# Optimization experiments

Measured on AMD Instinct MI355X. Metric: run time of the kernel, lower is better.

The kernel has to match this reference:

```python
import jax, jax.numpy as jnp
import numpy as np

VERY_NEG = -1e30


def setup_inputs() -> dict:
    key = jax.random.key(0)
    k1, k2, k3, k4, k5 = jax.random.split(key, 5)
    T, J, B, D = 1024, 128, 32, 256
    context = jax.random.normal(k1, (T, B, D), dtype=jnp.float32)
    question = jax.random.normal(k2, (J, B, D), dtype=jnp.float32)
    con_lens = jax.random.randint(k3, (B,), 1, T + 1)
    qu_lens = jax.random.randint(k4, (B,), 1, J + 1)
    # learned trilinear weight (3*D, 1), small init like uniform weight init
    att_w = jax.random.normal(k5, (3 * D, 1), dtype=jnp.float32) * 0.05
    return {"context": context, "question": question, "con_lens": con_lens,
            "qu_lens": qu_lens, "att_w": att_w}


def reference(context, question, con_lens, qu_lens, att_w):
    T, B, D = context.shape
    J = question.shape[0]
    # Decompose trilinear score: [c, q, c*q] @ att_w = c.w_c + q.w_q + (c*q).w_cq
    w_c, w_q, w_cq = att_w[:D, 0], att_w[D:2 * D, 0], att_w[2 * D:, 0]
    c_proj = jnp.einsum('tbd,d->bt', context, w_c)            # (B,T)
    q_proj = jnp.einsum('jbd,d->bj', question, w_q)           # (B,J)
    cross = jnp.einsum('tbd,jbd->btj', context * w_cq, question)  # (B,T,J)
    S = c_proj[:, :, None] + q_proj[:, None, :] + cross       # (B,T,J)
    # exp_mask: valid (t < con_len) & (j < qu_len), invalid += VERY_NEG
    t_valid = jnp.arange(T)[None, :] < con_lens[:, None]      # (B,T)
    j_valid = jnp.arange(J)[None, :] < qu_lens[:, None]       # (B,J)
    valid = t_valid[:, :, None] & j_valid[:, None, :]         # (B,T,J)
    S = S + jnp.where(valid, 0.0, VERY_NEG)
    # context-to-query attention
    c2q_w = jax.nn.softmax(S, axis=-1)                        # (B,T,J)
    question_bt = jnp.transpose(question, (1, 0, 2))          # (B,J,D)
    c2q = jnp.einsum('btj,bjd->btd', c2q_w, question_bt)      # (B,T,D)
    # query-to-context attention: rows of the expanded bmm are identical,
    # so compute the weighted sum once and broadcast (same math as expand+bmm)
    value = jax.nn.softmax(jnp.max(S, axis=2), axis=-1)       # (B,T)
    context_bt = jnp.transpose(context, (1, 0, 2))            # (B,T,D)
    q2c_vec = jnp.einsum('bt,btd->bd', value, context_bt)     # (B,D)
    q2c = jnp.broadcast_to(q2c_vec[:, None, :], (B, T, D))
    G = jnp.concatenate([context_bt, c2q, context_bt * c2q, context_bt * q2c],
                        axis=2)                               # (B,T,4D)
    # zero out padded context positions
    G = G * t_valid[:, :, None].astype(G.dtype)
    return G
```

## Files before the change

### kernel.cpp

```cpp
#include <hip/hip_runtime.h>
#include <hip/hip_bf16.h>

#define T_ 1024
#define J_ 128
#define B_ 32
#define D_ 256
#define VERY_NEG (-1e30f)

using u16 = unsigned short;
typedef __bf16 bf16x8 __attribute__((ext_vector_type(8)));
typedef u16 u16x8 __attribute__((ext_vector_type(8)));
typedef u16 u16x4 __attribute__((ext_vector_type(4)));
typedef float f32x4 __attribute__((ext_vector_type(4)));

__device__ __forceinline__ float bf2f(u16 u) {
  union { unsigned int i; float f; } v; v.i = ((unsigned int)u) << 16; return v.f;
}
__device__ __forceinline__ u16 f2bf(float f) {
  union { float f; unsigned int i; } v; v.f = f;
  unsigned int i = v.i;
  return (u16)((i + 0x7fffu + ((i >> 16) & 1u)) >> 16);
}

__global__ __launch_bounds__(256) void k_prep(const float* __restrict__ qst,
                                              const float* __restrict__ attw,
                                              float* __restrict__ ws_qproj,
                                              u16* __restrict__ ws_qbf) {
  const int wave = threadIdx.x >> 6, lane = threadIdx.x & 63;
  const int gid = blockIdx.x * 4 + wave;
  const int b = gid >> 7, j = gid & 127;
  const size_t off = (size_t)j * (B_ * D_) + b * D_ + lane * 4;
  f32x4 a = *(const f32x4*)(qst + off);
  f32x4 w = *(const f32x4*)(attw + D_ + lane * 4);
  u16x4 qb;
#pragma unroll
  for (int e = 0; e < 4; ++e) qb[e] = f2bf(a[e]);
  *(u16x4*)(ws_qbf + off) = qb;
  float s = a[0] * w[0] + a[1] * w[1] + a[2] * w[2] + a[3] * w[3];
#pragma unroll
  for (int m = 32; m >= 1; m >>= 1) s += __shfl_xor(s, m);
  if (lane == 0) ws_qproj[gid] = s;
}

__global__ __launch_bounds__(256) void k_main(const float* __restrict__ ctx,
                                              const u16* __restrict__ qbf,
                                              const int* __restrict__ con_lens,
                                              const int* __restrict__ qu_lens,
                                              const float* __restrict__ attw,
                                              const float* __restrict__ ws_qproj,
                                              float* __restrict__ ws_mtile,
                                              float* __restrict__ ws_pden,
                                              float* __restrict__ ws_pnum,
                                              float* __restrict__ out) {
  __shared__ __align__(16) u16 smem[24576];
  __shared__ float mrow_l[64];
  __shared__ float msc[1];
  u16* qtl = smem;
  u16* plds = smem + 16384;
  u16* c2q_l = smem;
  float* red4 = (float*)(smem + 16896);

  const int tid = threadIdx.x;
  const int wave = tid >> 6, lane = tid & 63;
  const int lrow = lane & 15, lgrp = lane >> 4;
  const int b = blockIdx.y;
  const int t0 = blockIdx.x * 64;
  const int t0w = t0 + wave * 16;
  const int con = con_lens[b], qu = qu_lens[b];

  f32x4 accS[8];
#pragma unroll
  for (int jb = 0; jb < 8; ++jb) accS[jb] = f32x4{0.f, 0.f, 0.f, 0.f};

  float cpr = 0.f;
  const float* rowAp = ctx + (size_t)(t0w + lrow) * (B_ * D_) + b * D_;
#pragma unroll
  for (int ks = 0; ks < 8; ++ks) {
    const int d0 = ks * 32 + lgrp * 8;
    f32x4 a0 = *(const f32x4*)(rowAp + d0);
    f32x4 a1 = *(const f32x4*)(rowAp + d0 + 4);
    f32x4 wq0 = *(const f32x4*)(attw + 2 * D_ + d0);
    f32x4 wq1 = *(const f32x4*)(attw + 2 * D_ + d0 + 4);
    f32x4 wc0 = *(const f32x4*)(attw + d0);
    f32x4 wc1 = *(const f32x4*)(attw + d0 + 4);
    bf16x8 afrag;
#pragma unroll
    for (int e = 0; e < 4; ++e) {
      afrag[e] = (__bf16)(a0[e] * wq0[e]);
      afrag[4 + e] = (__bf16)(a1[e] * wq1[e]);
      cpr += a0[e] * wc0[e] + a1[e] * wc1[e];
    }
#pragma unroll
    for (int jb = 0; jb < 8; ++jb) {
      const bf16x8 bfrag =
          *(const bf16x8*)(qbf + (size_t)(jb * 16 + lrow) * (B_ * D_) + b * D_ + d0);
      accS[jb] = __builtin_amdgcn_mfma_f32_16x16x32_bf16(afrag, bfrag, accS[jb], 0, 0, 0);
    }
  }
  cpr += __shfl_xor(cpr, 16);
  cpr += __shfl_xor(cpr, 32);

  float cp[4];
#pragma unroll
  for (int r = 0; r < 4; ++r) cp[r] = __shfl(cpr, lgrp * 4 + r);
  float qp[8];
#pragma unroll
  for (int jb = 0; jb < 8; ++jb) qp[jb] = ws_qproj[b * 128 + jb * 16 + lrow];

  float mx[4] = {-3e38f, -3e38f, -3e38f, -3e38f};
#pragma unroll
  for (int jb = 0; jb < 8; ++jb) {
    const int j = jb * 16 + lrow;
#pragma unroll
    for (int r = 0; r < 4; ++r) {
      const int t = t0w + lgrp * 4 + r;
      float s = accS[jb][r] + cp[r] + qp[jb];
      if (t >= con || j >= qu) s += VERY_NEG;
      accS[jb][r] = s;
      mx[r] = fmaxf(mx[r], s);
    }
  }
#pragma unroll
  for (int r = 0; r < 4; ++r) {
    mx[r] = fmaxf(mx[r], __shfl_xor(mx[r], 1));
    mx[r] = fmaxf(mx[r], __shfl_xor(mx[r], 2));
    mx[r] = fmaxf(mx[r], __shfl_xor(mx[r], 4));
    mx[r] = fmaxf(mx[r], __shfl_xor(mx[r], 8));
  }
  if (lrow == 0) {
#pragma unroll
    for (int r = 0; r < 4; ++r) mrow_l[wave * 16 + lgrp * 4 + r] = mx[r];
  }
  float sm[4] = {0.f, 0.f, 0.f, 0.f};
#pragma unroll
  for (int jb = 0; jb < 8; ++jb)
#pragma unroll
    for (int r = 0; r < 4; ++r) {
      float p = __expf(accS[jb][r] - mx[r]);
      accS[jb][r] = p;
      sm[r] += p;
    }
#pragma unroll
  for (int r = 0; r < 4; ++r) {
    sm[r] += __shfl_xor(sm[r], 1);
    sm[r] += __shfl_xor(sm[r], 2);
    sm[r] += __shfl_xor(sm[r], 4);
    sm[r] += __shfl_xor(sm[r], 8);
  }

  {
    u16* pl = plds + wave * 2048;
#pragma unroll
    for (int r = 0; r < 4; ++r) {
      const float inv = 1.0f / sm[r];
      const int m = lgrp * 4 + r;
#pragma unroll
      for (int jb = 0; jb < 8; ++jb) {
        const int n = jb * 16 + lrow;
        pl[m * 128 + (((n >> 3) ^ m) << 3) + (n & 7)] = f2bf(accS[jb][r] * inv);
      }
    }
  }

  f32x4 accO[16];
#pragma unroll
  for (int nb = 0; nb < 16; ++nb) accO[nb] = f32x4{0.f, 0.f, 0.f, 0.f};

#pragma unroll
  for (int h = 0; h < 2; ++h) {
    __syncthreads();
    for (int it = 0; it < 8; ++it) {
      const int task = it * 256 + tid;
      const int j = task & 127, dblk = task >> 7;
      u16x8 q = *(const u16x8*)(qbf + (size_t)j * (B_ * D_) + b * D_ + h * 128 + dblk * 8);
#pragma unroll
      for (int e = 0; e < 8; ++e) {
        const int dl = dblk * 8 + e;
        qtl[dl * 128 + (((j >> 3) ^ (dl & 15)) << 3) + (j & 7)] = q[e];
      }
    }
    __syncthreads();
#pragma unroll
    for (int ks2 = 0; ks2 < 4; ++ks2) {
      const int chunkA = ks2 * 4 + lgrp;
      const bf16x8 ap =
          *(const bf16x8*)(plds + wave * 2048 + lrow * 128 + ((chunkA ^ lrow) << 3));
#pragma unroll
      for (int nbl = 0; nbl < 8; ++nbl) {
        const int dl = nbl * 16 + lrow;
        const bf16x8 bq = *(const bf16x8*)(qtl + dl * 128 + ((chunkA ^ (dl & 15)) << 3));
        accO[h * 8 + nbl] =
            __builtin_amdgcn_mfma_f32_16x16x32_bf16(ap, bq, accO[h * 8 + nbl], 0, 0, 0);
      }
    }
  }
  __syncthreads();

#pragma unroll
  for (int nb = 0; nb < 16; ++nb)
#pragma unroll
    for (int r = 0; r < 4; ++r) {
      const int row = wave * 16 + lgrp * 4 + r;
      const int d = nb * 16 + lrow;
      c2q_l[row * 264 + d] = f2bf(accO[nb][r]);
    }
  __syncthreads();

  if (tid < 64) {
    float v = mrow_l[tid];
#pragma unroll
    for (int m = 32; m >= 1; m >>= 1) v = fmaxf(v, __shfl_xor(v, m));
    if (tid == 0) msc[0] = v;
  }
  __syncthreads();
  const float Mt = msc[0];
  if (tid < 64) {
    const float mr = mrow_l[tid];
    const float e = (mr < -1e29f) ? 0.f : __expf(mr - Mt);
    mrow_l[tid] = e;
    float s2 = e;
#pragma unroll
    for (int m = 32; m >= 1; m >>= 1) s2 += __shfl_xor(s2, m);
    if (tid == 0) {
      ws_mtile[b * 16 + blockIdx.x] = Mt;
      ws_pden[b * 16 + blockIdx.x] = s2;
    }
  }
  __syncthreads();

  f32x4 acc4 = {0.f, 0.f, 0.f, 0.f};
  const int c = tid & 63;
  for (int ii = 0; ii < 16; ++ii) {
    const int row = ii * 4 + wave;
    const int t = t0 + row;
    const bool valid = t < con;
    f32x4 cr = *(const f32x4*)(ctx + (size_t)t * (B_ * D_) + b * D_ + c * 4);
    u16x4 cq = *(const u16x4*)(c2q_l + row * 264 + c * 4);
    const float w = mrow_l[row];
    f32x4 p0, p1, p2;
#pragma unroll
    for (int e = 0; e < 4; ++e) {
      const float cf = valid ? cr[e] : 0.f;
      const float qf = valid ? bf2f(cq[e]) : 0.f;
      p0[e] = cf;
      p1[e] = qf;
      p2[e] = cf * qf;
      acc4[e] += w * cr[e];
    }
    float* g = out + ((size_t)(b * 1024 + t)) * 1024 + c * 4;
    *(f32x4*)(g) = p0;
    *(f32x4*)(g + 256) = p1;
    *(f32x4*)(g + 512) = p2;
  }
  *(f32x4*)(red4 + wave * 256 + c * 4) = acc4;
  __syncthreads();
  {
    const float sum = red4[tid] + red4[256 + tid] + red4[512 + tid] + red4[768 + tid];
    ws_pnum[((size_t)b * 16 + blockIdx.x) * 256 + tid] = sum;
  }
}

__global__ __launch_bounds__(256) void k_combine(const float* __restrict__ ws_mtile,
                                                 const float* __restrict__ ws_pden,
                                                 const float* __restrict__ ws_pnum,
                                                 float* __restrict__ q2c) {
  __shared__ float se[16];
  __shared__ float sden[1];
  const int b = blockIdx.x, tid = threadIdx.x;
  if (tid < 64) {
    const float mt = (tid < 16) ? ws_mtile[b * 16 + tid] : -3e38f;
    float M = mt;
#pragma unroll
    for (int m = 8; m >= 1; m >>= 1) M = fmaxf(M, __shfl_xor(M, m));
    const float pd = (tid < 16) ? ws_pden[b * 16 + tid] : 0.f;
    const float e = (tid < 16 && mt > -1e29f) ? __expf(mt - M) : 0.f;
    if (tid < 16) se[tid] = e;
    float cden = e * pd;
#pragma unroll
    for (int m = 8; m >= 1; m >>= 1) cden += __shfl_xor(cden, m);
    if (tid == 0) sden[0] = cden;
  }
  __syncthreads();
  const float den = sden[0];
  float num = 0.f;
#pragma unroll
  for (int i = 0; i < 16; ++i) num += se[i] * ws_pnum[((size_t)b * 16 + i) * 256 + tid];
  q2c[b * 256 + tid] = num / den;
}

__global__ __launch_bounds__(256) void k_part3(const float* __restrict__ ctx,
                                               const int* __restrict__ con_lens,
                                               const float* __restrict__ q2c,
                                               float* __restrict__ out) {
  const int idx = blockIdx.x * 256 + threadIdx.x;
  const int c = idx & 63, t = (idx >> 6) & 1023, b = idx >> 16;
  const bool valid = t < con_lens[b];
  f32x4 cr = *(const f32x4*)(ctx + (size_t)t * (B_ * D_) + b * D_ + c * 4);
  const f32x4 qv = *(const f32x4*)(q2c + b * D_ + c * 4);
  f32x4 o;
#pragma unroll
  for (int e = 0; e < 4; ++e) o[e] = valid ? cr[e] * qv[e] : 0.f;
  *(f32x4*)(out + ((size_t)(b * 1024 + t)) * 1024 + 768 + c * 4) = o;
}

extern "C" void kernel_launch(void* const* d_in, const int* in_sizes, int n_in,
                              void* d_out, int out_size, void* d_ws, size_t ws_size,
                              hipStream_t stream) {
  const float* ctx = (const float*)d_in[0];
  const float* qst = (const float*)d_in[1];
  const int* con = (const int*)d_in[2];
  const int* qu = (const int*)d_in[3];
  const float* attw = (const float*)d_in[4];
  float* out = (float*)d_out;

  float* ws = (float*)d_ws;
  float* ws_qproj = ws;
  u16* ws_qbf = (u16*)(ws + 4096);
  float* ws_mtile = ws + 528384;
  float* ws_pden = ws + 528896;
  float* ws_pnum = ws + 529408;
  float* ws_q2c = ws + 660480;

  k_prep<<<1024, 256, 0, stream>>>(qst, attw, ws_qproj, ws_qbf);
  k_main<<<dim3(16, 32), 256, 0, stream>>>(ctx, ws_qbf, con, qu, attw, ws_qproj,
                                           ws_mtile, ws_pden, ws_pnum, out);
  k_combine<<<32, 256, 0, stream>>>(ws_mtile, ws_pden, ws_pnum, ws_q2c);
  k_part3<<<8192, 256, 0, stream>>>(ctx, con, ws_q2c, out);
}
```

Measured before the change: 190.7 us.

## Fuse all stages into one kernel with per-batch spin barriers

Merges prep, main, combine and the q2c output pass into a single persistent kernel. Per-batch global atomic counters act as barriers between the 16 blocks of each batch. Context rows stay in registers so the q2c output columns are written without re-reading ctx, and three kernel launches go away. The cost is a memset per call, spin-wait barriers that depend on all 512 blocks being co-resident (launch bounds 256,2), and more register pressure from caching 16 f32x4 values.

```diff
diff --git a/kernel.cpp b/kernel.cpp
--- a/kernel.cpp
+++ b/kernel.cpp
@@ -22,39 +22,32 @@
   return (u16)((i + 0x7fffu + ((i >> 16) & 1u)) >> 16);
 }
 
-__global__ __launch_bounds__(256) void k_prep(const float* __restrict__ qst,
-                                              const float* __restrict__ attw,
-                                              float* __restrict__ ws_qproj,
-                                              u16* __restrict__ ws_qbf) {
-  const int wave = threadIdx.x >> 6, lane = threadIdx.x & 63;
-  const int gid = blockIdx.x * 4 + wave;
-  const int b = gid >> 7, j = gid & 127;
-  const size_t off = (size_t)j * (B_ * D_) + b * D_ + lane * 4;
-  f32x4 a = *(const f32x4*)(qst + off);
-  f32x4 w = *(const f32x4*)(attw + D_ + lane * 4);
-  u16x4 qb;
-#pragma unroll
-  for (int e = 0; e < 4; ++e) qb[e] = f2bf(a[e]);
-  *(u16x4*)(ws_qbf + off) = qb;
-  float s = a[0] * w[0] + a[1] * w[1] + a[2] * w[2] + a[3] * w[3];
-#pragma unroll
-  for (int m = 32; m >= 1; m >>= 1) s += __shfl_xor(s, m);
-  if (lane == 0) ws_qproj[gid] = s;
-}
-
-__global__ __launch_bounds__(256) void k_main(const float* __restrict__ ctx,
-                                              const u16* __restrict__ qbf,
-                                              const int* __restrict__ con_lens,
-                                              const int* __restrict__ qu_lens,
-                                              const float* __restrict__ attw,
-                                              const float* __restrict__ ws_qproj,
-                                              float* __restrict__ ws_mtile,
-                                              float* __restrict__ ws_pden,
-                                              float* __restrict__ ws_pnum,
-                                              float* __restrict__ out) {
+__device__ __forceinline__ void b_barrier(int* cnt, int tid) {
+  __threadfence();
+  __syncthreads();
+  if (tid == 0) {
+    __hip_atomic_fetch_add(cnt, 1, __ATOMIC_RELEASE, __HIP_MEMORY_SCOPE_AGENT);
+    while (__hip_atomic_load(cnt, __ATOMIC_ACQUIRE, __HIP_MEMORY_SCOPE_AGENT) < 16) {
+      __builtin_amdgcn_s_sleep(1);
+    }
+  }
+  __syncthreads();
+  __threadfence();
+}
+
+__global__ __launch_bounds__(256, 2) void k_fused(
+    const float* __restrict__ ctx, const float* __restrict__ qst,
+    const int* __restrict__ con_lens, const int* __restrict__ qu_lens,
+    const float* __restrict__ attw, float* __restrict__ ws_qproj,
+    u16* __restrict__ ws_qbf, float* __restrict__ ws_mtile,
+    float* __restrict__ ws_pden, float* __restrict__ ws_pnum,
+    int* __restrict__ ws_cnt, float* __restrict__ out) {
   __shared__ __align__(16) u16 smem[24576];
   __shared__ float mrow_l[64];
   __shared__ float msc[1];
+  __shared__ float se_s[16];
+  __shared__ float den_s[1];
+  __shared__ float q2c_l[256];
   u16* qtl = smem;
   u16* plds = smem + 16384;
   u16* c2q_l = smem;
@@ -67,6 +60,23 @@
   const int t0 = blockIdx.x * 64;
   const int t0w = t0 + wave * 16;
   const int con = con_lens[b], qu = qu_lens[b];
+
+#pragma unroll
+  for (int h = 0; h < 2; ++h) {
+    const int j = blockIdx.x * 8 + wave * 2 + h;
+    const size_t off = (size_t)j * (B_ * D_) + b * D_ + lane * 4;
+    f32x4 a = *(const f32x4*)(qst + off);
+    f32x4 w = *(const f32x4*)(attw + D_ + lane * 4);
+    u16x4 qb;
+#pragma unroll
+    for (int e = 0; e < 4; ++e) qb[e] = f2bf(a[e]);
+    *(u16x4*)(ws_qbf + off) = qb;
+    float s = a[0] * w[0] + a[1] * w[1] + a[2] * w[2] + a[3] * w[3];
+#pragma unroll
+    for (int m = 32; m >= 1; m >>= 1) s += __shfl_xor(s, m);
+    if (lane == 0) ws_qproj[b * 128 + j] = s;
+  }
+  b_barrier(&ws_cnt[b], tid);
 
   f32x4 accS[8];
 #pragma unroll
@@ -93,7 +103,7 @@
 #pragma unroll
     for (int jb = 0; jb < 8; ++jb) {
       const bf16x8 bfrag =
-          *(const bf16x8*)(qbf + (size_t)(jb * 16 + lrow) * (B_ * D_) + b * D_ + d0);
+          *(const bf16x8*)(ws_qbf + (size_t)(jb * 16 + lrow) * (B_ * D_) + b * D_ + d0);
       accS[jb] = __builtin_amdgcn_mfma_f32_16x16x32_bf16(afrag, bfrag, accS[jb], 0, 0, 0);
     }
   }
@@ -172,7 +182,8 @@
     for (int it = 0; it < 8; ++it) {
       const int task = it * 256 + tid;
       const int j = task & 127, dblk = task >> 7;
-      u16x8 q = *(const u16x8*)(qbf + (size_t)j * (B_ * D_) + b * D_ + h * 128 + dblk * 8);
+      u16x8 q =
+          *(const u16x8*)(ws_qbf + (size_t)j * (B_ * D_) + b * D_ + h * 128 + dblk * 8);
 #pragma unroll
       for (int e = 0; e < 8; ++e) {
         const int dl = dblk * 8 + e;
@@ -228,24 +239,26 @@
   }
   __syncthreads();
 
+  f32x4 cr[16];
   f32x4 acc4 = {0.f, 0.f, 0.f, 0.f};
   const int c = tid & 63;
+#pragma unroll
   for (int ii = 0; ii < 16; ++ii) {
     const int row = ii * 4 + wave;
     const int t = t0 + row;
     const bool valid = t < con;
-    f32x4 cr = *(const f32x4*)(ctx + (size_t)t * (B_ * D_) + b * D_ + c * 4);
+    cr[ii] = *(const f32x4*)(ctx + (size_t)t * (B_ * D_) + b * D_ + c * 4);
     u16x4 cq = *(const u16x4*)(c2q_l + row * 264 + c * 4);
     const float w = mrow_l[row];
     f32x4 p0, p1, p2;
 #pragma unroll
     for (int e = 0; e < 4; ++e) {
-      const float cf = valid ? cr[e] : 0.f;
+      const float cf = valid ? cr[ii][e] : 0.f;
       const float qf = valid ? bf2f(cq[e]) : 0.f;
       p0[e] = cf;
       p1[e] = qf;
       p2[e] = cf * qf;
-      acc4[e] += w * cr[e];
+      acc4[e] += w * cr[ii][e];
     }
     float* g = out + ((size_t)(b * 1024 + t)) * 1024 + c * 4;
     *(f32x4*)(g) = p0;
@@ -254,53 +267,54 @@
   }
   *(f32x4*)(red4 + wave * 256 + c * 4) = acc4;
   __syncthreads();
+  ws_pnum[((size_t)b * 16 + blockIdx.x) * 256 + tid] =
+      red4[tid] + red4[256 + tid] + red4[512 + tid] + red4[768 + tid];
+
+  b_barrier(&ws_cnt[B_ + b], tid);
+
+  if (tid < 64) {
+    const float mt = (tid < 16)
+        ? __hip_atomic_load(&ws_mtile[b * 16 + tid], __ATOMIC_RELAXED,
+                            __HIP_MEMORY_SCOPE_AGENT)
+        : -3e38f;
+    float M = mt;
+#pragma unroll
+    for (int m = 8; m >= 1; m >>= 1) M = fmaxf(M, __shfl_xor(M, m));
+    const float pd = (tid < 16)
+        ? __hip_atomic_load(&ws_pden[b * 16 + tid], __ATOMIC_RELAXED,
+                            __HIP_MEMORY_SCOPE_AGENT)
+        : 0.f;
+    const float e = (tid < 16 && mt > -1e29f) ? __expf(mt - M) : 0.f;
+    if (tid < 16) se_s[tid] = e;
+    float cden = e * pd;
+#pragma unroll
+    for (int m = 8; m >= 1; m >>= 1) cden += __shfl_xor(cden, m);
+    if (tid == 0) den_s[0] = cden;
+  }
+  __syncthreads();
   {
-    const float sum = red4[tid] + red4[256 + tid] + red4[512 + tid] + red4[768 + tid];
-    ws_pnum[((size_t)b * 16 + blockIdx.x) * 256 + tid] = sum;
-  }
-}
-
-__global__ __launch_bounds__(256) void k_combine(const float* __restrict__ ws_mtile,
-                                                 const float* __restrict__ ws_pden,
-                                                 const float* __restrict__ ws_pnum,
-                                                 float* __restrict__ q2c) {
-  __shared__ float se[16];
-  __shared__ float sden[1];
-  const int b = blockIdx.x, tid = threadIdx.x;
-  if (tid < 64) {
-    const float mt = (tid < 16) ? ws_mtile[b * 16 + tid] : -3e38f;
-    float M = mt;
-#pragma unroll
-    for (int m = 8; m >= 1; m >>= 1) M = fmaxf(M, __shfl_xor(M, m));
-    const float pd = (tid < 16) ? ws_pden[b * 16 + tid] : 0.f;
-    const float e = (tid < 16 && mt > -1e29f) ? __expf(mt - M) : 0.f;
-    if (tid < 16) se[tid] = e;
-    float cden = e * pd;
-#pragma unroll
-    for (int m = 8; m >= 1; m >>= 1) cden += __shfl_xor(cden, m);
-    if (tid == 0) sden[0] = cden;
-  }
-  __syncthreads();
-  const float den = sden[0];
-  float num = 0.f;
-#pragma unroll
-  for (int i = 0; i < 16; ++i) num += se[i] * ws_pnum[((size_t)b * 16 + i) * 256 + tid];
-  q2c[b * 256 + tid] = num / den;
-}
-
-__global__ __launch_bounds__(256) void k_part3(const float* __restrict__ ctx,
-                                               const int* __restrict__ con_lens,
-                                               const float* __restrict__ q2c,
-                                               float* __restrict__ out) {
-  const int idx = blockIdx.x * 256 + threadIdx.x;
-  const int c = idx & 63, t = (idx >> 6) & 1023, b = idx >> 16;
-  const bool valid = t < con_lens[b];
-  f32x4 cr = *(const f32x4*)(ctx + (size_t)t * (B_ * D_) + b * D_ + c * 4);
-  const f32x4 qv = *(const f32x4*)(q2c + b * D_ + c * 4);
-  f32x4 o;
-#pragma unroll
-  for (int e = 0; e < 4; ++e) o[e] = valid ? cr[e] * qv[e] : 0.f;
-  *(f32x4*)(out + ((size_t)(b * 1024 + t)) * 1024 + 768 + c * 4) = o;
+    float num = 0.f;
+#pragma unroll
+    for (int i = 0; i < 16; ++i) {
+      const float pn = __hip_atomic_load(&ws_pnum[((size_t)b * 16 + i) * 256 + tid],
+                                         __ATOMIC_RELAXED, __HIP_MEMORY_SCOPE_AGENT);
+      num += se_s[i] * pn;
+    }
+    q2c_l[tid] = num / den_s[0];
+  }
+  __syncthreads();
+
+  const f32x4 qv = *(const f32x4*)(q2c_l + c * 4);
+#pragma unroll
+  for (int ii = 0; ii < 16; ++ii) {
+    const int row = ii * 4 + wave;
+    const int t = t0 + row;
+    const bool valid = t < con;
+    f32x4 o;
+#pragma unroll
+    for (int e = 0; e < 4; ++e) o[e] = valid ? cr[ii][e] * qv[e] : 0.f;
+    *(f32x4*)(out + ((size_t)(b * 1024 + t)) * 1024 + 768 + c * 4) = o;
+  }
 }
 
 extern "C" void kernel_launch(void* const* d_in, const int* in_sizes, int n_in,
@@ -319,11 +333,9 @@
   float* ws_mtile = ws + 528384;
   float* ws_pden = ws + 528896;
   float* ws_pnum = ws + 529408;
-  float* ws_q2c = ws + 660480;
-
-  k_prep<<<1024, 256, 0, stream>>>(qst, attw, ws_qproj, ws_qbf);
-  k_main<<<dim3(16, 32), 256, 0, stream>>>(ctx, ws_qbf, con, qu, attw, ws_qproj,
-                                           ws_mtile, ws_pden, ws_pnum, out);
-  k_combine<<<32, 256, 0, stream>>>(ws_mtile, ws_pden, ws_pnum, ws_q2c);
-  k_part3<<<8192, 256, 0, stream>>>(ctx, con, ws_q2c, out);
-}
+  int* ws_cnt = (int*)(ws + 660480);
+
+  hipMemsetAsync((void*)ws_cnt, 0, 64 * sizeof(int), stream);
+  k_fused<<<dim3(16, 32), 256, 0, stream>>>(ctx, qst, con, qu, attw, ws_qproj, ws_qbf,
+                                            ws_mtile, ws_pden, ws_pnum, ws_cnt, out);
+}
```

Result: slower. 481.0 us (+152.3%).
